# Kernel optimization log

Hardware: AMD Instinct MI355X
Metric: run time of the kernel (lower is better)

## Reference

```python
import jax, jax.numpy as jnp
import numpy as np

B, S, D = 128, 8192, 64  # batch, source_length, bin_rep_size (32 * 2 directions)

def setup_inputs() -> dict:
    key = jax.random.key(0)
    kx, kv = jax.random.split(key)
    x = jax.random.normal(kx, (B, S, D), dtype=jnp.float32)
    # original uses tf.random.uniform((bin_rep_size, 1))
    v = jax.random.uniform(kv, (D, 1), dtype=jnp.float32)
    return {"x": x, "v": v}

def reference(x, v):
    # scores: batched matvec against the context vector -> [B, S]
    scores = jnp.einsum('bsd,dk->bs', x, v)
    # softmax over source_length (axis=1 in original)
    alpha = jax.nn.softmax(scores, axis=1)          # [B, S]
    alpha = alpha[:, None, :]                        # [B, 1, S]
    out = jnp.matmul(alpha, x)                       # [B, 1, D]
    return (out, alpha)
```

## Files before the change

### kernel.cpp

```cpp
#include <hip/hip_runtime.h>
#include <math.h>

#define BB 128
#define SS 8192
#define DD 64
#define KP 8
#define ROWS_PER_BLOCK (SS / KP)
#define THREADS 512
#define NWAVES (THREADS / 64)
#define UNROLL 8

__device__ __forceinline__ float row_sum16(float x) {
    int t;
    t = __builtin_amdgcn_update_dpp(0, __float_as_int(x), 0xB1, 0xF, 0xF, true);
    x += __int_as_float(t);
    t = __builtin_amdgcn_update_dpp(0, __float_as_int(x), 0x4E, 0xF, 0xF, true);
    x += __int_as_float(t);
    t = __builtin_amdgcn_update_dpp(0, __float_as_int(x), 0x141, 0xF, 0xF, true);
    x += __int_as_float(t);
    t = __builtin_amdgcn_update_dpp(0, __float_as_int(x), 0x140, 0xF, 0xF, true);
    x += __int_as_float(t);
    return x;
}

__global__ __launch_bounds__(THREADS) void k1_partial(
    const float* __restrict__ x, const float* __restrict__ v,
    float* __restrict__ alpha_out,
    float* __restrict__ acc_p,
    float* __restrict__ l_p)
{
    const int blk  = blockIdx.x;
    const int b    = blk / KP;
    const int p    = blk % KP;
    const int tid  = threadIdx.x;
    const int wave = tid >> 6;
    const int lane = tid & 63;
    const int q    = lane & 15;
    const int r    = lane >> 4;

    const float4 v4 = ((const float4*)v)[q];

    const int rows_per_wave = ROWS_PER_BLOCK / NWAVES;
    const int iters         = rows_per_wave / 4;
    const int s_base        = p * ROWS_PER_BLOCK + wave * rows_per_wave;
    const float* xb = x + (size_t)b * SS * DD;

    float4 acc = make_float4(0.f, 0.f, 0.f, 0.f);
    float lsum = 0.f;

    for (int i0 = 0; i0 < iters; i0 += UNROLL) {
        float4 xs[UNROLL];
        #pragma unroll
        for (int u = 0; u < UNROLL; ++u) {
            const int srow = s_base + (i0 + u) * 4;
            xs[u] = ((const float4*)(xb + (size_t)srow * DD))[lane];
        }
        #pragma unroll
        for (int u = 0; u < UNROLL; ++u) {
            const int srow = s_base + (i0 + u) * 4;
            const float4 x4 = xs[u];
            float sc = x4.x * v4.x + x4.y * v4.y + x4.z * v4.z + x4.w * v4.w;
            sc = row_sum16(sc);
            const float w = __expf(sc);
            if (q == 0) {
                alpha_out[(size_t)b * SS + srow + r] = w;
                lsum += w;
            }
            acc.x += w * x4.x;
            acc.y += w * x4.y;
            acc.z += w * x4.z;
            acc.w += w * x4.w;
        }
    }

    acc.x += __shfl_xor(acc.x, 16); acc.x += __shfl_xor(acc.x, 32);
    acc.y += __shfl_xor(acc.y, 16); acc.y += __shfl_xor(acc.y, 32);
    acc.z += __shfl_xor(acc.z, 16); acc.z += __shfl_xor(acc.z, 32);
    acc.w += __shfl_xor(acc.w, 16); acc.w += __shfl_xor(acc.w, 32);
    lsum  += __shfl_xor(lsum, 16);  lsum  += __shfl_xor(lsum, 32);

    __shared__ float s_acc[NWAVES][DD];
    __shared__ float s_l[NWAVES];
    if (r == 0) {
        ((float4*)s_acc[wave])[q] = acc;
        if (q == 0) s_l[wave] = lsum;
    }
    __syncthreads();

    if (tid < DD) {
        float a = 0.f;
        #pragma unroll
        for (int w = 0; w < NWAVES; ++w) a += s_acc[w][tid];
        acc_p[((size_t)b * KP + p) * DD + tid] = a;
    }
    if (tid == 0) {
        float l = 0.f;
        #pragma unroll
        for (int w = 0; w < NWAVES; ++w) l += s_l[w];
        l_p[b * KP + p] = l;
    }
}

__global__ __launch_bounds__(DD) void k2_combine(
    const float* __restrict__ acc_p, const float* __restrict__ l_p,
    float* __restrict__ out, float* __restrict__ inv_l)
{
    const int b = blockIdx.x;
    const int d = threadIdx.x;
    float a = 0.f;
    #pragma unroll
    for (int p = 0; p < KP; ++p) a += acc_p[((size_t)b * KP + p) * DD + d];
    float l = 0.f;
    #pragma unroll
    for (int p = 0; p < KP; ++p) l += l_p[b * KP + p];
    const float il = 1.0f / l;
    out[b * DD + d] = a * il;
    if (d == 0) inv_l[b] = il;
}

__global__ __launch_bounds__(256) void k3_scale(
    float* __restrict__ alpha, const float* __restrict__ inv_l)
{
    const int idx = blockIdx.x * 256 + threadIdx.x;
    const int b = idx >> 13;
    alpha[idx] *= inv_l[b];
}

extern "C" void kernel_launch(void* const* d_in, const int* in_sizes, int n_in,
                              void* d_out, int out_size, void* d_ws, size_t ws_size,
                              hipStream_t stream) {
    const float* x = (const float*)d_in[0];
    const float* v = (const float*)d_in[1];

    float* out   = (float*)d_out;
    float* alpha = (float*)d_out + BB * DD;

    float* acc_p = (float*)d_ws;
    float* l_p   = acc_p + BB * KP * DD;
    float* inv_l = l_p + BB * KP;

    k1_partial<<<BB * KP, THREADS, 0, stream>>>(x, v, alpha, acc_p, l_p);
    k2_combine<<<BB, DD, 0, stream>>>(acc_p, l_p, out, inv_l);
    k3_scale<<<(BB * SS) / 256, 256, 0, stream>>>(alpha, inv_l);
}
```

Before: 352.6 us.

## Interleave row tiles across waves with per-batch phase; vectorize alpha scaling

The main kernel now gives each wave 32 four-row tiles strided across the whole sequence, instead of one contiguous chunk of rows. The starting tile is rotated by the batch index so that concurrent blocks hit different address ranges, which should spread DRAM channel traffic. The scaling kernel now handles four alpha values per thread with float4 loads and stores, cutting thread count and instruction overhead. The strided access gives up per-wave contiguity, which may hurt prefetch or row-buffer locality.

```diff
diff --git a/kernel.cpp b/kernel.cpp
--- a/kernel.cpp
+++ b/kernel.cpp
@@ -5,9 +5,10 @@
 #define SS 8192
 #define DD 64
 #define KP 8
-#define ROWS_PER_BLOCK (SS / KP)
 #define THREADS 512
 #define NWAVES (THREADS / 64)
+#define WPB 64
+#define TILES_PER_WAVE 32
 #define UNROLL 8
 
 __device__ __forceinline__ float row_sum16(float x) {
@@ -37,33 +38,33 @@
     const int lane = tid & 63;
     const int q    = lane & 15;
     const int r    = lane >> 4;
+    const int wg   = p * NWAVES + wave;
+    const int phase = b & 31;
 
     const float4 v4 = ((const float4*)v)[q];
-
-    const int rows_per_wave = ROWS_PER_BLOCK / NWAVES;
-    const int iters         = rows_per_wave / 4;
-    const int s_base        = p * ROWS_PER_BLOCK + wave * rows_per_wave;
     const float* xb = x + (size_t)b * SS * DD;
+    float* ab = alpha_out + (size_t)b * SS;
 
     float4 acc = make_float4(0.f, 0.f, 0.f, 0.f);
     float lsum = 0.f;
 
-    for (int i0 = 0; i0 < iters; i0 += UNROLL) {
+    for (int i0 = 0; i0 < TILES_PER_WAVE; i0 += UNROLL) {
         float4 xs[UNROLL];
+        int rows[UNROLL];
         #pragma unroll
         for (int u = 0; u < UNROLL; ++u) {
-            const int srow = s_base + (i0 + u) * 4;
-            xs[u] = ((const float4*)(xb + (size_t)srow * DD))[lane];
+            const int tile = ((i0 + u + phase) & 31) * WPB + wg;
+            rows[u] = tile * 4;
+            xs[u] = ((const float4*)(xb + (size_t)rows[u] * DD))[lane];
         }
         #pragma unroll
         for (int u = 0; u < UNROLL; ++u) {
-            const int srow = s_base + (i0 + u) * 4;
             const float4 x4 = xs[u];
             float sc = x4.x * v4.x + x4.y * v4.y + x4.z * v4.z + x4.w * v4.w;
             sc = row_sum16(sc);
             const float w = __expf(sc);
             if (q == 0) {
-                alpha_out[(size_t)b * SS + srow + r] = w;
+                ab[rows[u] + r] = w;
                 lsum += w;
             }
             acc.x += w * x4.x;
@@ -121,9 +122,12 @@
 __global__ __launch_bounds__(256) void k3_scale(
     float* __restrict__ alpha, const float* __restrict__ inv_l)
 {
-    const int idx = blockIdx.x * 256 + threadIdx.x;
-    const int b = idx >> 13;
-    alpha[idx] *= inv_l[b];
+    const int i4 = blockIdx.x * 256 + threadIdx.x;
+    const int b  = i4 >> 11;
+    const float il = inv_l[b];
+    float4 a = ((float4*)alpha)[i4];
+    a.x *= il; a.y *= il; a.z *= il; a.w *= il;
+    ((float4*)alpha)[i4] = a;
 }
 
 extern "C" void kernel_launch(void* const* d_in, const int* in_sizes, int n_in,
@@ -141,5 +145,5 @@
 
     k1_partial<<<BB * KP, THREADS, 0, stream>>>(x, v, alpha, acc_p, l_p);
     k2_combine<<<BB, DD, 0, stream>>>(acc_p, l_p, out, inv_l);
-    k3_scale<<<(BB * SS) / 256, 256, 0, stream>>>(alpha, inv_l);
+    k3_scale<<<(BB * SS) / (256 * 4), 256, 0, stream>>>(alpha, inv_l);
 }
```

Measured after the change: 352.3 us. No clear change (-0.1%).

## Stage alpha in LDS, interleave rows across waves, fuse combine and scale kernels

Applied to the files above, without the earlier changes.

The partial kernel now uses smaller blocks (512 rows, 256 threads, 16 partitions per batch) with rows interleaved across waves. It buffers the unnormalized weights in shared memory and writes them to global memory as coalesced float2 stores, replacing the scattered per-row stores. The separate combine and scale kernels are merged into one per-batch kernel that reduces the partials and rescales alpha with float4 accesses, removing one launch and the inv_l round trip. The cost is fewer blocks in the finishing stage (128) and twice as many partials to reduce.

```diff
diff --git a/kernel.cpp b/kernel.cpp
--- a/kernel.cpp
+++ b/kernel.cpp
@@ -4,11 +4,12 @@
 #define BB 128
 #define SS 8192
 #define DD 64
-#define KP 8
-#define ROWS_PER_BLOCK (SS / KP)
-#define THREADS 512
-#define NWAVES (THREADS / 64)
-#define UNROLL 8
+#define RPB 512
+#define KP (SS / RPB)
+#define THREADS 256
+#define NWAVES 4
+#define STEPS (RPB / 16)
+#define UNROLL 4
 
 __device__ __forceinline__ float row_sum16(float x) {
     int t;
@@ -39,31 +40,29 @@
     const int r    = lane >> 4;
 
     const float4 v4 = ((const float4*)v)[q];
+    const float4* xb4 = (const float4*)(x + (size_t)b * SS * DD);
+    int idx4 = (p * RPB + wave * 4 + r) * 16 + q;
 
-    const int rows_per_wave = ROWS_PER_BLOCK / NWAVES;
-    const int iters         = rows_per_wave / 4;
-    const int s_base        = p * ROWS_PER_BLOCK + wave * rows_per_wave;
-    const float* xb = x + (size_t)b * SS * DD;
+    __shared__ __align__(16) float s_w[RPB];
+    __shared__ float s_acc[NWAVES][DD];
+    __shared__ float s_l[NWAVES];
 
     float4 acc = make_float4(0.f, 0.f, 0.f, 0.f);
     float lsum = 0.f;
 
-    for (int i0 = 0; i0 < iters; i0 += UNROLL) {
+    for (int i0 = 0; i0 < STEPS; i0 += UNROLL) {
         float4 xs[UNROLL];
         #pragma unroll
-        for (int u = 0; u < UNROLL; ++u) {
-            const int srow = s_base + (i0 + u) * 4;
-            xs[u] = ((const float4*)(xb + (size_t)srow * DD))[lane];
-        }
+        for (int u = 0; u < UNROLL; ++u)
+            xs[u] = xb4[(size_t)idx4 + (i0 + u) * 256];
         #pragma unroll
         for (int u = 0; u < UNROLL; ++u) {
-            const int srow = s_base + (i0 + u) * 4;
             const float4 x4 = xs[u];
             float sc = x4.x * v4.x + x4.y * v4.y + x4.z * v4.z + x4.w * v4.w;
             sc = row_sum16(sc);
             const float w = __expf(sc);
             if (q == 0) {
-                alpha_out[(size_t)b * SS + srow + r] = w;
+                s_w[(i0 + u) * 16 + wave * 4 + r] = w;
                 lsum += w;
             }
             acc.x += w * x4.x;
@@ -79,13 +78,14 @@
     acc.w += __shfl_xor(acc.w, 16); acc.w += __shfl_xor(acc.w, 32);
     lsum  += __shfl_xor(lsum, 16);  lsum  += __shfl_xor(lsum, 32);
 
-    __shared__ float s_acc[NWAVES][DD];
-    __shared__ float s_l[NWAVES];
     if (r == 0) {
         ((float4*)s_acc[wave])[q] = acc;
         if (q == 0) s_l[wave] = lsum;
     }
     __syncthreads();
+
+    float* ab = alpha_out + (size_t)b * SS + p * RPB;
+    ((float2*)ab)[tid] = ((const float2*)s_w)[tid];
 
     if (tid < DD) {
         float a = 0.f;
@@ -101,29 +101,33 @@
     }
 }
 
-__global__ __launch_bounds__(DD) void k2_combine(
+__global__ __launch_bounds__(THREADS) void k2_finish(
     const float* __restrict__ acc_p, const float* __restrict__ l_p,
-    float* __restrict__ out, float* __restrict__ inv_l)
+    float* __restrict__ out, float* __restrict__ alpha)
 {
     const int b = blockIdx.x;
-    const int d = threadIdx.x;
-    float a = 0.f;
-    #pragma unroll
-    for (int p = 0; p < KP; ++p) a += acc_p[((size_t)b * KP + p) * DD + d];
+    const int tid = threadIdx.x;
+
     float l = 0.f;
     #pragma unroll
     for (int p = 0; p < KP; ++p) l += l_p[b * KP + p];
     const float il = 1.0f / l;
-    out[b * DD + d] = a * il;
-    if (d == 0) inv_l[b] = il;
-}
 
-__global__ __launch_bounds__(256) void k3_scale(
-    float* __restrict__ alpha, const float* __restrict__ inv_l)
-{
-    const int idx = blockIdx.x * 256 + threadIdx.x;
-    const int b = idx >> 13;
-    alpha[idx] *= inv_l[b];
+    if (tid < DD) {
+        float a = 0.f;
+        #pragma unroll
+        for (int p = 0; p < KP; ++p) a += acc_p[((size_t)b * KP + p) * DD + tid];
+        out[b * DD + tid] = a * il;
+    }
+
+    float4* ab4 = (float4*)(alpha + (size_t)b * SS);
+    #pragma unroll
+    for (int j = 0; j < (SS / 4) / THREADS; ++j) {
+        const int idx = j * THREADS + tid;
+        float4 a = ab4[idx];
+        a.x *= il; a.y *= il; a.z *= il; a.w *= il;
+        ab4[idx] = a;
+    }
 }
 
 extern "C" void kernel_launch(void* const* d_in, const int* in_sizes, int n_in,
@@ -137,9 +141,7 @@
 
     float* acc_p = (float*)d_ws;
     float* l_p   = acc_p + BB * KP * DD;
-    float* inv_l = l_p + BB * KP;
 
     k1_partial<<<BB * KP, THREADS, 0, stream>>>(x, v, alpha, acc_p, l_p);
-    k2_combine<<<BB, DD, 0, stream>>>(acc_p, l_p, out, inv_l);
-    k3_scale<<<(BB * SS) / 256, 256, 0, stream>>>(alpha, inv_l);
+    k2_finish<<<BB, THREADS, 0, stream>>>(acc_p, l_p, out, alpha);
 }
```

Result: no change. 357.8 us (+1.5%).
